# Kernel tuning notes

Hardware: AMD Instinct MI355X
Metric: run time of the kernel (lower is better)

Reference implementation:

```python
import jax, jax.numpy as jnp
import numpy as np
from jax import lax

B = 32        # true batch size (groups)
C_IN = 64     # per-sample input channels
C_OUT = 64    # per-sample output channels
H = W = 256
KH = KW = 3


def setup_inputs() -> dict:
    key = jax.random.key(0)
    kx, kk = jax.random.split(key)
    # x folds the batch into channels: [1, B*C_in, H, W]
    x = jax.random.normal(kx, (1, B * C_IN, H, W), dtype=jnp.float32)
    # per-sample kernels stacked along output-filter axis: [B*C_out, C_in, kH, kW]
    kernels = jax.random.normal(kk, (B * C_OUT, C_IN, KH, KW), dtype=jnp.float32)
    return {"x": x, "kernels": kernels, "batch_size": B}


def reference(x, kernels, batch_size):
    # F.conv2d(x, kernels, stride=1, padding='same', groups=batch_size)
    # Grouped conv with feature_group_count = batch_size (one group per sample).
    out = lax.conv_general_dilated(
        x,
        kernels,
        window_strides=(1, 1),
        padding="SAME",
        feature_group_count=batch_size,
        dimension_numbers=("NCHW", "OIHW", "NCHW"),
    )
    return out
```

## Files before the change

kernel.cpp:

```cpp
#include <hip/hip_runtime.h>
#include <hip/hip_bf16.h>


typedef __bf16 bf16x8 __attribute__((ext_vector_type(8)));
typedef float  f32x4  __attribute__((ext_vector_type(4)));

#define NB 32
#define NH 256
#define NW 256
#define TILE_H 4
#define TILE_W 64
#define XROWS 6
#define XCOLS 68

__global__ void repack_weights_kernel(const float* __restrict__ wsrc,
                                      __bf16* __restrict__ pk) {
    int t = blockIdx.x * blockDim.x + threadIdx.x;
    if (t >= NB * 9 * 4 * 2 * 64) return;
    int lane = t & 63;
    int r = t >> 6;
    int kc = r & 1;  r >>= 1;
    int mt = r & 3;  r >>= 2;
    int tap = r % 9;
    int b   = r / 9;
    int co  = b * 64 + mt * 16 + (lane & 15);
    int ci0 = kc * 32 + (lane >> 4) * 8;
    bf16x8 v;
#pragma unroll
    for (int j = 0; j < 8; ++j) {
        v[j] = (__bf16)wsrc[(co * 64 + ci0 + j) * 9 + tap];
    }
    *reinterpret_cast<bf16x8*>(pk + (size_t)t * 8) = v;
}

__launch_bounds__(256)
__global__ void conv_mfma_kernel(const float* __restrict__ x,
                                 const __bf16* __restrict__ pk,
                                 float* __restrict__ out) {
    __shared__ __align__(16) __bf16 xs[XROWS * XCOLS * 32];

    const int orig = blockIdx.x;
    const int wg   = (orig & 7) * 1024 + (orig >> 3);
    const int b    = wg >> 8;
    const int by   = (wg >> 2) & 63;
    const int bx   = wg & 3;
    const int h0   = by * TILE_H;
    const int w0   = bx * TILE_W;

    const int tid  = threadIdx.x;
    const int wid  = tid >> 6;
    const int lane = tid & 63;
    const int nl   = lane & 15;
    const int kgrp = lane >> 4;

    const __bf16* pkb = pk + (size_t)b * 9 * 4096;

    bf16x8 af[4][4];
    auto load_af = [&](int g) {
        const int tap = (g >= 9) ? g - 9 : g;
        const int kc  = (g >= 9) ? 1 : 0;
        const int sl  = g & 3;
#pragma unroll
        for (int mt = 0; mt < 4; ++mt)
            af[sl][mt] = *reinterpret_cast<const bf16x8*>(
                pkb + tap * 4096 + ((mt * 2 + kc) * 64 + lane) * 8);
    };

    load_af(0);
    load_af(1);

    f32x4 acc[4][4];
#pragma unroll
    for (int mt = 0; mt < 4; ++mt)
#pragma unroll
        for (int q = 0; q < 4; ++q)
            acc[mt][q] = (f32x4){0.f, 0.f, 0.f, 0.f};

    const int c    = lane;
    const int w    = w0 - 1 + c;
    const int wcl  = min(max(w, 0), NW - 1);
    const bool wbad = (w != wcl);
    const int sciw = ((wid ^ ((c >> 1) & 3)) * 8);

    const int hidx  = tid;
    const int hr    = hidx >> 3;
    const int hside = (hidx >> 2) & 1;
    const int hoct  = hidx & 3;
    const int hch   = 64 + hside;
    const int hw    = w0 + 63 + hside;
    const int hwc   = min(hw, NW - 1);

#pragma unroll
    for (int kc = 0; kc < 2; ++kc) {
        {
            const int cibase = b * 64 + kc * 32 + wid * 8;
            const float* colp = x + (size_t)cibase * NH * NW + wcl;

            float hv[8];
            if (tid < 48) {
                const int h  = h0 - 1 + hr;
                const int hc = min(max(h, 0), NH - 1);
                const float* src = x + ((size_t)(b * 64 + kc * 32 + hoct * 8) * NH + hc) * NW + hwc;
#pragma unroll
                for (int j = 0; j < 8; ++j) hv[j] = src[(size_t)j * NH * NW];
                if (h != hc || hw != hwc) {
#pragma unroll
                    for (int j = 0; j < 8; ++j) hv[j] = 0.f;
                }
            }

            float va[8], vb[8];
            auto load8 = [&](int r, float* v) {
                const int h  = h0 - 1 + r;
                const int hc = min(max(h, 0), NH - 1);
                const float* src = colp + (size_t)hc * NW;
#pragma unroll
                for (int j = 0; j < 8; ++j) v[j] = src[(size_t)j * NH * NW];
                if (wbad || h != hc) {
#pragma unroll
                    for (int j = 0; j < 8; ++j) v[j] = 0.f;
                }
            };
            auto store8 = [&](int r, const float* v) {
                bf16x8 o;
#pragma unroll
                for (int j = 0; j < 8; ++j) o[j] = (__bf16)v[j];
                *reinterpret_cast<bf16x8*>(xs + (r * XCOLS + c) * 32 + sciw) = o;
            };

            load8(0, va);
            load8(1, vb);
            store8(0, va); load8(2, va);
            store8(1, vb); load8(3, vb);
            store8(2, va); load8(4, va);
            store8(3, vb); load8(5, vb);
            store8(4, va);
            store8(5, vb);

            if (tid < 48) {
                bf16x8 o;
#pragma unroll
                for (int j = 0; j < 8; ++j) o[j] = (__bf16)hv[j];
                *reinterpret_cast<bf16x8*>(xs + (hr * XCOLS + hch) * 32 + hoct * 8) = o;
            }
        }
        __syncthreads();

#pragma unroll
        for (int tap = 0; tap < 9; ++tap) {
            const int g = kc * 9 + tap;
            if (g + 2 < 18) load_af(g + 2);
            const int kh = tap / 3;
            const int kw = tap - kh * 3;
            const int rowbase = (wid + kh) * XCOLS;
            const int fs = g & 3;
#pragma unroll
            for (int q = 0; q < 4; ++q) {
                const int cc   = q * 16 + nl + kw;
                const int slot = (cc >> 1) & 3;
                bf16x8 bfv = *reinterpret_cast<const bf16x8*>(
                    xs + (rowbase + cc) * 32 + ((kgrp ^ slot) * 8));
#pragma unroll
                for (int mt = 0; mt < 4; ++mt)
                    acc[mt][q] = __builtin_amdgcn_mfma_f32_16x16x32_bf16(
                        af[fs][mt], bfv, acc[mt][q], 0, 0, 0);
            }
        }
        if (kc == 0) __syncthreads();
    }

    const int mrow = kgrp * 4;
    const int h = h0 + wid;
#pragma unroll
    for (int mt = 0; mt < 4; ++mt) {
#pragma unroll
        for (int q = 0; q < 4; ++q) {
            const int ww = w0 + q * 16 + nl;
#pragma unroll
            for (int rg = 0; rg < 4; ++rg) {
                const int co = mt * 16 + mrow + rg;
                out[((size_t)(b * 64 + co) * NH + h) * NW + ww] = acc[mt][q][rg];
            }
        }
    }
}

extern "C" void kernel_launch(void* const* d_in, const int* in_sizes, int n_in,
                              void* d_out, int out_size, void* d_ws, size_t ws_size,
                              hipStream_t stream) {
    const float* x = (const float*)d_in[0];
    const float* w = (const float*)d_in[1];
    float* out = (float*)d_out;
    __bf16* pk = (__bf16*)d_ws;

    {
        int total = NB * 9 * 4 * 2 * 64;
        int blk = 256;
        int grid = (total + blk - 1) / blk;
        hipLaunchKernelGGL(repack_weights_kernel, dim3(grid), dim3(blk), 0, stream,
                           w, pk);
    }
    {
        dim3 grid(8192);
        hipLaunchKernelGGL(conv_mfma_kernel, grid, dim3(256), 0, stream,
                           x, pk, out);
    }
}
```

Measured before the change: 311.6 us.

## Double output tile height to 8 rows with 512-thread blocks

Each workgroup now covers 8 output rows instead of 4, using 8 waves and a 10-row shared-memory halo tile. Two groups of four waves each load 5 rows per channel octet. This cuts the halo re-read overhead from 6/4 to 10/8 rows loaded per output row and halves the number of workgroups. In exchange, LDS use per block grows and occupancy may change with the larger blocks.

```diff
diff --git a/kernel.cpp b/kernel.cpp
--- a/kernel.cpp
+++ b/kernel.cpp
@@ -8,10 +8,11 @@
 #define NB 32
 #define NH 256
 #define NW 256
-#define TILE_H 4
+#define TILE_H 8
 #define TILE_W 64
-#define XROWS 6
+#define XROWS 10
 #define XCOLS 68
+#define HWSZ ((size_t)NH * NW)
 
 __global__ void repack_weights_kernel(const float* __restrict__ wsrc,
                                       __bf16* __restrict__ pk) {
@@ -33,16 +34,16 @@
     *reinterpret_cast<bf16x8*>(pk + (size_t)t * 8) = v;
 }
 
-__launch_bounds__(256)
+__launch_bounds__(512)
 __global__ void conv_mfma_kernel(const float* __restrict__ x,
                                  const __bf16* __restrict__ pk,
                                  float* __restrict__ out) {
     __shared__ __align__(16) __bf16 xs[XROWS * XCOLS * 32];
 
     const int orig = blockIdx.x;
-    const int wg   = (orig & 7) * 1024 + (orig >> 3);
-    const int b    = wg >> 8;
-    const int by   = (wg >> 2) & 63;
+    const int wg   = (orig & 7) * 512 + (orig >> 3);
+    const int b    = wg >> 7;
+    const int by   = (wg >> 2) & 31;
     const int bx   = wg & 3;
     const int h0   = by * TILE_H;
     const int w0   = bx * TILE_W;
@@ -76,16 +77,17 @@
         for (int q = 0; q < 4; ++q)
             acc[mt][q] = (f32x4){0.f, 0.f, 0.f, 0.f};
 
-    const int c    = lane;
-    const int w    = w0 - 1 + c;
-    const int wcl  = min(max(w, 0), NW - 1);
+    const int c     = lane;
+    const int w     = w0 - 1 + c;
+    const int wcl   = min(max(w, 0), NW - 1);
     const bool wbad = (w != wcl);
-    const int sciw = ((wid ^ ((c >> 1) & 3)) * 8);
-
-    const int hidx  = tid;
-    const int hr    = hidx >> 3;
-    const int hside = (hidx >> 2) & 1;
-    const int hoct  = hidx & 3;
+    const int oct   = wid & 3;
+    const int rbase = (wid >> 2) * 5;
+    const int sciw  = ((oct ^ ((c >> 1) & 3)) * 8);
+
+    const int hr    = tid >> 3;
+    const int hside = (tid >> 2) & 1;
+    const int hoct  = tid & 3;
     const int hch   = 64 + hside;
     const int hw    = w0 + 63 + hside;
     const int hwc   = min(hw, NW - 1);
@@ -93,51 +95,52 @@
 #pragma unroll
     for (int kc = 0; kc < 2; ++kc) {
         {
-            const int cibase = b * 64 + kc * 32 + wid * 8;
-            const float* colp = x + (size_t)cibase * NH * NW + wcl;
+            const int cibase = b * 64 + kc * 32 + oct * 8;
+            const float* colp = x + (size_t)cibase * HWSZ + wcl;
 
             float hv[8];
-            if (tid < 48) {
+            if (tid < 80) {
                 const int h  = h0 - 1 + hr;
                 const int hc = min(max(h, 0), NH - 1);
                 const float* src = x + ((size_t)(b * 64 + kc * 32 + hoct * 8) * NH + hc) * NW + hwc;
 #pragma unroll
-                for (int j = 0; j < 8; ++j) hv[j] = src[(size_t)j * NH * NW];
+                for (int j = 0; j < 8; ++j) hv[j] = src[j * HWSZ];
                 if (h != hc || hw != hwc) {
 #pragma unroll
                     for (int j = 0; j < 8; ++j) hv[j] = 0.f;
                 }
             }
 
-            float va[8], vb[8];
+            float va[8], vb[8], vc[8];
             auto load8 = [&](int r, float* v) {
-                const int h  = h0 - 1 + r;
+                const int h  = h0 - 1 + rbase + r;
                 const int hc = min(max(h, 0), NH - 1);
                 const float* src = colp + (size_t)hc * NW;
 #pragma unroll
-                for (int j = 0; j < 8; ++j) v[j] = src[(size_t)j * NH * NW];
+                for (int j = 0; j < 8; ++j) v[j] = src[j * HWSZ];
                 if (wbad || h != hc) {
 #pragma unroll
                     for (int j = 0; j < 8; ++j) v[j] = 0.f;
                 }
             };
             auto store8 = [&](int r, const float* v) {
+                const int rr = rbase + r;
                 bf16x8 o;
 #pragma unroll
                 for (int j = 0; j < 8; ++j) o[j] = (__bf16)v[j];
-                *reinterpret_cast<bf16x8*>(xs + (r * XCOLS + c) * 32 + sciw) = o;
+                *reinterpret_cast<bf16x8*>(xs + (rr * XCOLS + c) * 32 + sciw) = o;
             };
 
             load8(0, va);
             load8(1, vb);
-            store8(0, va); load8(2, va);
-            store8(1, vb); load8(3, vb);
-            store8(2, va); load8(4, va);
-            store8(3, vb); load8(5, vb);
-            store8(4, va);
-            store8(5, vb);
-
-            if (tid < 48) {
+            load8(2, vc);
+            store8(0, va); load8(3, va);
+            store8(1, vb); load8(4, vb);
+            store8(2, vc);
+            store8(3, va);
+            store8(4, vb);
+
+            if (tid < 80) {
                 bf16x8 o;
 #pragma unroll
                 for (int j = 0; j < 8; ++j) o[j] = (__bf16)hv[j];
@@ -201,8 +204,8 @@
                            w, pk);
     }
     {
-        dim3 grid(8192);
-        hipLaunchKernelGGL(conv_mfma_kernel, grid, dim3(256), 0, stream,
+        dim3 grid(4096);
+        hipLaunchKernelGGL(conv_mfma_kernel, grid, dim3(512), 0, stream,
                            x, pk, out);
     }
 }
```

Measured after the change: 319.2 us. 1.02x slower.

## Stage input tiles via async global-to-LDS loads overlapped with MFMA compute

Applied to the files above, without the earlier changes.

Input rows are now fetched with global_load_lds DMA into an fp32 LDS scratch buffer, then converted to bf16 into the swizzled tile. The second channel-half load is issued partway through the first half's MFMA loop, so it overlaps with compute. The halo columns are loaded separately into registers. This adds 48KB of LDS scratch, which may reduce occupancy, and relies on the compiler and hardware ordering the async LDS writes before the barrier.

```diff
diff --git a/kernel.cpp b/kernel.cpp
--- a/kernel.cpp
+++ b/kernel.cpp
@@ -12,6 +12,15 @@
 #define TILE_W 64
 #define XROWS 6
 #define XCOLS 68
+#define HWSZ ((size_t)NH * NW)
+
+template<int P> struct IC { static constexpr int v = P; };
+
+__device__ __forceinline__ void gload16(const float* g, float* lds) {
+    __builtin_amdgcn_global_load_lds(
+        (const __attribute__((address_space(1))) unsigned int*)g,
+        (__attribute__((address_space(3))) unsigned int*)lds, 16, 0, 0);
+}
 
 __global__ void repack_weights_kernel(const float* __restrict__ wsrc,
                                       __bf16* __restrict__ pk) {
@@ -38,6 +47,7 @@
                                  const __bf16* __restrict__ pk,
                                  float* __restrict__ out) {
     __shared__ __align__(16) __bf16 xs[XROWS * XCOLS * 32];
+    __shared__ __align__(16) float  scratch[XROWS * 32 * 64];
 
     const int orig = blockIdx.x;
     const int wg   = (orig & 7) * 1024 + (orig >> 3);
@@ -66,9 +76,6 @@
                 pkb + tap * 4096 + ((mt * 2 + kc) * 64 + lane) * 8);
     };
 
-    load_af(0);
-    load_af(1);
-
     f32x4 acc[4][4];
 #pragma unroll
     for (int mt = 0; mt < 4; ++mt)
@@ -76,80 +83,76 @@
         for (int q = 0; q < 4; ++q)
             acc[mt][q] = (f32x4){0.f, 0.f, 0.f, 0.f};
 
-    const int c    = lane;
-    const int w    = w0 - 1 + c;
-    const int wcl  = min(max(w, 0), NW - 1);
-    const bool wbad = (w != wcl);
-    const int sciw = ((wid ^ ((c >> 1) & 3)) * 8);
-
-    const int hidx  = tid;
-    const int hr    = hidx >> 3;
-    const int hside = (hidx >> 2) & 1;
-    const int hoct  = hidx & 3;
-    const int hch   = 64 + hside;
-    const int hw    = w0 + 63 + hside;
-    const int hwc   = min(hw, NW - 1);
-
-#pragma unroll
-    for (int kc = 0; kc < 2; ++kc) {
-        {
-            const int cibase = b * 64 + kc * 32 + wid * 8;
-            const float* colp = x + (size_t)cibase * NH * NW + wcl;
-
-            float hv[8];
-            if (tid < 48) {
-                const int h  = h0 - 1 + hr;
-                const int hc = min(max(h, 0), NH - 1);
-                const float* src = x + ((size_t)(b * 64 + kc * 32 + hoct * 8) * NH + hc) * NW + hwc;
-#pragma unroll
-                for (int j = 0; j < 8; ++j) hv[j] = src[(size_t)j * NH * NW];
-                if (h != hc || hw != hwc) {
-#pragma unroll
-                    for (int j = 0; j < 8; ++j) hv[j] = 0.f;
-                }
+    const int hside = tid & 1;
+    const int hidx  = tid >> 1;
+    const int hrr   = hidx % 6;
+    const int hoo   = hidx / 6;
+    const int hch   = hside ? 65 : 0;
+    const int hwv   = hside ? (w0 + 64) : (w0 - 1);
+    float hreg[8];
+    bool  hz = false;
+
+    auto issue_gload = [&](int kcv) {
+#pragma unroll
+        for (int m = 0; m < 12; ++m) {
+            const int I  = wid * 12 + m;
+            const int r  = I >> 3;
+            const int cb = I & 7;
+            const int hh = h0 - 1 + r;
+            const int hc = min(max(hh, 0), NH - 1);
+            const float* src = x
+                + ((size_t)(b * 64 + kcv * 32 + cb * 4 + (lane >> 4)) * NH + hc) * NW
+                + w0 + (lane & 15) * 4;
+            gload16(src, scratch + (r * 32 + cb * 4) * 64);
+        }
+    };
+
+    auto issue_halo = [&](int kcv) {
+        if (tid < 48) {
+            const int hh = h0 - 1 + hrr;
+            hz = (hwv < 0) || (hwv > NW - 1) || (hh < 0) || (hh > NH - 1);
+            const int wc2 = min(max(hwv, 0), NW - 1);
+            const int hc2 = min(max(hh, 0), NH - 1);
+            const float* s = x + ((size_t)(b * 64 + kcv * 32 + hoo * 8) * NH + hc2) * NW + wc2;
+#pragma unroll
+            for (int j = 0; j < 8; ++j) hreg[j] = s[j * HWSZ];
+        }
+    };
+
+    auto cvt = [&]() {
+#pragma unroll
+        for (int rr = 0; rr < XROWS; ++rr) {
+            const int hh = h0 - 1 + rr;
+            const bool z = (hh < 0) || (hh > NH - 1);
+            float v[8];
+#pragma unroll
+            for (int j = 0; j < 8; ++j)
+                v[j] = scratch[(rr * 32 + wid * 8 + j) * 64 + lane];
+            bf16x8 o8;
+#pragma unroll
+            for (int j = 0; j < 8; ++j) o8[j] = z ? (__bf16)0.f : (__bf16)v[j];
+            const int c = lane + 1;
+            *reinterpret_cast<bf16x8*>(
+                xs + (rr * XCOLS + c) * 32 + ((wid ^ ((c >> 1) & 3)) * 8)) = o8;
+        }
+        if (tid < 48) {
+            bf16x8 o8;
+#pragma unroll
+            for (int j = 0; j < 8; ++j) o8[j] = hz ? (__bf16)0.f : (__bf16)hreg[j];
+            *reinterpret_cast<bf16x8*>(xs + (hrr * XCOLS + hch) * 32 + hoo * 8) = o8;
+        }
+    };
+
+    auto comp = [&](auto parc, auto issc) {
+        constexpr int PAR = decltype(parc)::v;
+        constexpr int ISS = decltype(issc)::v;
+#pragma unroll
+        for (int tap = 0; tap < 9; ++tap) {
+            const int g = PAR * 9 + tap;
+            if (g + 2 < 18) load_af(g + 2);
+            if constexpr (ISS) {
+                if (tap == 3) { issue_gload(1); issue_halo(1); }
             }
-
-            float va[8], vb[8];
-            auto load8 = [&](int r, float* v) {
-                const int h  = h0 - 1 + r;
-                const int hc = min(max(h, 0), NH - 1);
-                const float* src = colp + (size_t)hc * NW;
-#pragma unroll
-                for (int j = 0; j < 8; ++j) v[j] = src[(size_t)j * NH * NW];
-                if (wbad || h != hc) {
-#pragma unroll
-                    for (int j = 0; j < 8; ++j) v[j] = 0.f;
-                }
-            };
-            auto store8 = [&](int r, const float* v) {
-                bf16x8 o;
-#pragma unroll
-                for (int j = 0; j < 8; ++j) o[j] = (__bf16)v[j];
-                *reinterpret_cast<bf16x8*>(xs + (r * XCOLS + c) * 32 + sciw) = o;
-            };
-
-            load8(0, va);
-            load8(1, vb);
-            store8(0, va); load8(2, va);
-            store8(1, vb); load8(3, vb);
-            store8(2, va); load8(4, va);
-            store8(3, vb); load8(5, vb);
-            store8(4, va);
-            store8(5, vb);
-
-            if (tid < 48) {
-                bf16x8 o;
-#pragma unroll
-                for (int j = 0; j < 8; ++j) o[j] = (__bf16)hv[j];
-                *reinterpret_cast<bf16x8*>(xs + (hr * XCOLS + hch) * 32 + hoct * 8) = o;
-            }
-        }
-        __syncthreads();
-
-#pragma unroll
-        for (int tap = 0; tap < 9; ++tap) {
-            const int g = kc * 9 + tap;
-            if (g + 2 < 18) load_af(g + 2);
             const int kh = tap / 3;
             const int kw = tap - kh * 3;
             const int rowbase = (wid + kh) * XCOLS;
@@ -166,8 +169,20 @@
                         af[fs][mt], bfv, acc[mt][q], 0, 0, 0);
             }
         }
-        if (kc == 0) __syncthreads();
-    }
+    };
+
+    load_af(0);
+    load_af(1);
+    issue_gload(0);
+    issue_halo(0);
+    __syncthreads();
+    cvt();
+    __syncthreads();
+    comp(IC<0>{}, IC<1>{});
+    __syncthreads();
+    cvt();
+    __syncthreads();
+    comp(IC<1>{}, IC<0>{});
 
     const int mrow = kgrp * 4;
     const int h = h0 + wid;
```

Result: slower. 323.8 us (+3.9%).

## Halve output tile height and split channels across waves for occupancy

Applied to the files above, without the earlier changes.

The output tile shrinks from 4 rows to 2 rows, and the grid doubles. Each pair of waves now shares one output row, with each wave computing half of the 64 output channels. This halves the accumulator and weight-fragment registers and adds a min-waves hint of 5, so more workgroups can be resident per CU. In exchange, halo overhead grows: 4 staged rows per 2 output rows instead of 6 per 4. The input reads, redundant halo loads and weight-fragment loads per output all rise.

```diff
diff --git a/kernel.cpp b/kernel.cpp
--- a/kernel.cpp
+++ b/kernel.cpp
@@ -8,10 +8,11 @@
 #define NB 32
 #define NH 256
 #define NW 256
-#define TILE_H 4
+#define TILE_H 2
 #define TILE_W 64
-#define XROWS 6
-#define XCOLS 68
+#define XROWS 4
+#define XCOLS 66
+#define HWSZ ((size_t)NH * NW)
 
 __global__ void repack_weights_kernel(const float* __restrict__ wsrc,
                                       __bf16* __restrict__ pk) {
@@ -33,16 +34,16 @@
     *reinterpret_cast<bf16x8*>(pk + (size_t)t * 8) = v;
 }
 
-__launch_bounds__(256)
+__launch_bounds__(256, 5)
 __global__ void conv_mfma_kernel(const float* __restrict__ x,
                                  const __bf16* __restrict__ pk,
                                  float* __restrict__ out) {
     __shared__ __align__(16) __bf16 xs[XROWS * XCOLS * 32];
 
     const int orig = blockIdx.x;
-    const int wg   = (orig & 7) * 1024 + (orig >> 3);
-    const int b    = wg >> 8;
-    const int by   = (wg >> 2) & 63;
+    const int wg   = (orig & 7) * 2048 + (orig >> 3);
+    const int b    = wg >> 9;
+    const int by   = (wg >> 2) & 127;
     const int bx   = wg & 3;
     const int h0   = by * TILE_H;
     const int w0   = bx * TILE_W;
@@ -52,40 +53,43 @@
     const int lane = tid & 63;
     const int nl   = lane & 15;
     const int kgrp = lane >> 4;
+    const int rloc = wid >> 1;
+    const int ch   = wid & 1;
 
     const __bf16* pkb = pk + (size_t)b * 9 * 4096;
 
-    bf16x8 af[4][4];
+    bf16x8 af[4][2];
     auto load_af = [&](int g) {
         const int tap = (g >= 9) ? g - 9 : g;
         const int kc  = (g >= 9) ? 1 : 0;
         const int sl  = g & 3;
 #pragma unroll
-        for (int mt = 0; mt < 4; ++mt)
-            af[sl][mt] = *reinterpret_cast<const bf16x8*>(
-                pkb + tap * 4096 + ((mt * 2 + kc) * 64 + lane) * 8);
+        for (int mtl = 0; mtl < 2; ++mtl) {
+            const int mtg = ch * 2 + mtl;
+            af[sl][mtl] = *reinterpret_cast<const bf16x8*>(
+                pkb + tap * 4096 + ((mtg * 2 + kc) * 64 + lane) * 8);
+        }
     };
-
     load_af(0);
     load_af(1);
 
-    f32x4 acc[4][4];
-#pragma unroll
-    for (int mt = 0; mt < 4; ++mt)
+    f32x4 acc[2][4];
+#pragma unroll
+    for (int mtl = 0; mtl < 2; ++mtl)
 #pragma unroll
         for (int q = 0; q < 4; ++q)
-            acc[mt][q] = (f32x4){0.f, 0.f, 0.f, 0.f};
+            acc[mtl][q] = (f32x4){0.f, 0.f, 0.f, 0.f};
 
     const int c    = lane;
     const int w    = w0 - 1 + c;
     const int wcl  = min(max(w, 0), NW - 1);
     const bool wbad = (w != wcl);
-    const int sciw = ((wid ^ ((c >> 1) & 3)) * 8);
-
-    const int hidx  = tid;
-    const int hr    = hidx >> 3;
-    const int hside = (hidx >> 2) & 1;
-    const int hoct  = hidx & 3;
+    const int oct  = wid;
+    const int sciw = ((oct ^ ((c >> 1) & 3)) * 8);
+
+    const int hr    = tid >> 3;
+    const int hside = (tid >> 2) & 1;
+    const int hoct  = tid & 3;
     const int hch   = 64 + hside;
     const int hw    = w0 + 63 + hside;
     const int hwc   = min(hw, NW - 1);
@@ -93,16 +97,16 @@
 #pragma unroll
     for (int kc = 0; kc < 2; ++kc) {
         {
-            const int cibase = b * 64 + kc * 32 + wid * 8;
-            const float* colp = x + (size_t)cibase * NH * NW + wcl;
+            const int cibase = b * 64 + kc * 32 + oct * 8;
+            const float* colp = x + (size_t)cibase * HWSZ + wcl;
 
             float hv[8];
-            if (tid < 48) {
+            if (tid < 32) {
                 const int h  = h0 - 1 + hr;
                 const int hc = min(max(h, 0), NH - 1);
                 const float* src = x + ((size_t)(b * 64 + kc * 32 + hoct * 8) * NH + hc) * NW + hwc;
 #pragma unroll
-                for (int j = 0; j < 8; ++j) hv[j] = src[(size_t)j * NH * NW];
+                for (int j = 0; j < 8; ++j) hv[j] = src[j * HWSZ];
                 if (h != hc || hw != hwc) {
 #pragma unroll
                     for (int j = 0; j < 8; ++j) hv[j] = 0.f;
@@ -115,7 +119,7 @@
                 const int hc = min(max(h, 0), NH - 1);
                 const float* src = colp + (size_t)hc * NW;
 #pragma unroll
-                for (int j = 0; j < 8; ++j) v[j] = src[(size_t)j * NH * NW];
+                for (int j = 0; j < 8; ++j) v[j] = src[j * HWSZ];
                 if (wbad || h != hc) {
 #pragma unroll
                     for (int j = 0; j < 8; ++j) v[j] = 0.f;
@@ -132,12 +136,10 @@
             load8(1, vb);
             store8(0, va); load8(2, va);
             store8(1, vb); load8(3, vb);
-            store8(2, va); load8(4, va);
-            store8(3, vb); load8(5, vb);
-            store8(4, va);
-            store8(5, vb);
-
-            if (tid < 48) {
+            store8(2, va);
+            store8(3, vb);
+
+            if (tid < 32) {
                 bf16x8 o;
 #pragma unroll
                 for (int j = 0; j < 8; ++j) o[j] = (__bf16)hv[j];
@@ -152,7 +154,7 @@
             if (g + 2 < 18) load_af(g + 2);
             const int kh = tap / 3;
             const int kw = tap - kh * 3;
-            const int rowbase = (wid + kh) * XCOLS;
+            const int rowbase = (rloc + kh) * XCOLS;
             const int fs = g & 3;
 #pragma unroll
             for (int q = 0; q < 4; ++q) {
@@ -161,25 +163,25 @@
                 bf16x8 bfv = *reinterpret_cast<const bf16x8*>(
                     xs + (rowbase + cc) * 32 + ((kgrp ^ slot) * 8));
 #pragma unroll
-                for (int mt = 0; mt < 4; ++mt)
-                    acc[mt][q] = __builtin_amdgcn_mfma_f32_16x16x32_bf16(
-                        af[fs][mt], bfv, acc[mt][q], 0, 0, 0);
+                for (int mtl = 0; mtl < 2; ++mtl)
+                    acc[mtl][q] = __builtin_amdgcn_mfma_f32_16x16x32_bf16(
+                        af[fs][mtl], bfv, acc[mtl][q], 0, 0, 0);
             }
         }
         if (kc == 0) __syncthreads();
     }
 
     const int mrow = kgrp * 4;
-    const int h = h0 + wid;
-#pragma unroll
-    for (int mt = 0; mt < 4; ++mt) {
+    const int h = h0 + rloc;
+#pragma unroll
+    for (int mtl = 0; mtl < 2; ++mtl) {
 #pragma unroll
         for (int q = 0; q < 4; ++q) {
             const int ww = w0 + q * 16 + nl;
 #pragma unroll
             for (int rg = 0; rg < 4; ++rg) {
-                const int co = mt * 16 + mrow + rg;
-                out[((size_t)(b * 64 + co) * NH + h) * NW + ww] = acc[mt][q][rg];
+                const int co = (ch * 2 + mtl) * 16 + mrow + rg;
+                out[((size_t)(b * 64 + co) * NH + h) * NW + ww] = acc[mtl][q][rg];
             }
         }
     }
@@ -201,7 +203,7 @@
                            w, pk);
     }
     {
-        dim3 grid(8192);
+        dim3 grid(16384);
         hipLaunchKernelGGL(conv_mfma_kernel, grid, dim3(256), 0, stream,
                            x, pk, out);
     }
```

New measurement: 667.5 us. 2.14x slower.
